# Kernel tuning notes

Measured on AMD Instinct MI355X. Metric: run time of the kernel, lower is better.

Reference implementation:

```python
import jax, jax.numpy as jnp
import numpy as np

B, S, D, H = 2, 2048, 1024, 16
DK = D // H


def setup_inputs() -> dict:
    key = jax.random.key(0)
    ks = jax.random.split(key, 11)
    scale = 1.0 / np.sqrt(D)
    inp = {
        "query": jax.random.normal(ks[0], (B, S, D), dtype=jnp.float32),
        "key": jax.random.normal(ks[1], (B, S, D), dtype=jnp.float32),
        "value": jax.random.normal(ks[2], (B, S, D), dtype=jnp.float32),
        "Wq": jax.random.normal(ks[3], (D, D), dtype=jnp.float32) * scale,
        "bq": jnp.zeros((D,), dtype=jnp.float32),
        "Wk": jax.random.normal(ks[4], (D, D), dtype=jnp.float32) * scale,
        "bk": jnp.zeros((D,), dtype=jnp.float32),
        "Wv": jax.random.normal(ks[5], (D, D), dtype=jnp.float32) * scale,
        "bv": jnp.zeros((D,), dtype=jnp.float32),
        "Wo": jax.random.normal(ks[6], (D, D), dtype=jnp.float32) * scale,
        "bo": jnp.zeros((D,), dtype=jnp.float32),
    }
    return inp


def _split_heads(x):
    # [B,S,D] -> [B,H,S,DK]
    b, s, _ = x.shape
    return x.reshape(b, s, H, DK).transpose(0, 2, 1, 3)


def reference(query, key, value, Wq, bq, Wk, bk, Wv, bv, Wo, bo):
    q = _split_heads(query @ Wq.T + bq)
    k = _split_heads(key @ Wk.T + bk)
    v = _split_heads(value @ Wv.T + bv)
    # scaled dot-product attention: [B,H,S,S]
    scores = jnp.einsum("bhqd,bhkd->bhqk", q, k) / np.sqrt(DK).astype(np.float32)
    attn = jax.nn.softmax(scores, axis=-1)  # stable max-subtract softmax, same math
    ctx = jnp.einsum("bhqk,bhkd->bhqd", attn, v)  # [B,H,S,DK]
    ctx = ctx.transpose(0, 2, 1, 3).reshape(query.shape[0], -1, H * DK)
    return ctx @ Wo.T + bo
```

## Files before the change

kernel.cpp:

```cpp
#include <hip/hip_runtime.h>
#include <math.h>

constexpr int NB = 2;
constexpr int NS = 2048;
constexpr int ND = 1024;
constexpr int NH = 16;
constexpr int NDK = 64;

typedef __attribute__((ext_vector_type(8))) short short8;
typedef __attribute__((ext_vector_type(4))) float floatx4;

__device__ inline unsigned short f2bf(float x) {
    unsigned u = __builtin_bit_cast(unsigned, x);
    u += 0x7fffu + ((u >> 16) & 1u);
    return (unsigned short)(u >> 16);
}

__device__ inline uint4 pack8(float4 a, float4 b) {
    unsigned short t[8] = {f2bf(a.x), f2bf(a.y), f2bf(a.z), f2bf(a.w),
                           f2bf(b.x), f2bf(b.y), f2bf(b.z), f2bf(b.w)};
    return *(uint4*)t;
}

#define GLOAD_LDS16(g, l) __builtin_amdgcn_global_load_lds( \
    (const __attribute__((address_space(1))) void*)(g),     \
    (__attribute__((address_space(3))) void*)(l), 16, 0, 0)

#define QSCALE 0.18033688f

__global__ __launch_bounds__(256) void cvt_all(
    const float* __restrict__ s0, const float* __restrict__ s1,
    const float* __restrict__ s2, const float* __restrict__ s3,
    const float* __restrict__ s4, const float* __restrict__ s5,
    const float* __restrict__ s6,
    unsigned short* __restrict__ d0, unsigned short* __restrict__ d1,
    unsigned short* __restrict__ d2, unsigned short* __restrict__ d3,
    unsigned short* __restrict__ d4, unsigned short* __restrict__ d5,
    unsigned short* __restrict__ d6)
{
    const int y = blockIdx.y;
    const float* srcs[7] = {s0, s1, s2, s3, s4, s5, s6};
    unsigned short* dsts[7] = {d0, d1, d2, d3, d4, d5, d6};
    const int nel = (y < 3) ? NB * NS * ND : ND * ND;
    int i = (blockIdx.x * 256 + threadIdx.x) * 8;
    if (i >= nel) return;
    const float* s = srcs[y];
    unsigned short* d = dsts[y];
    float4 a = *(const float4*)(s + i);
    float4 b = *(const float4*)(s + i + 4);
    *(uint4*)(d + i) = pack8(a, b);
}

__global__ __launch_bounds__(256) void gemm_qkv(
    const unsigned short* __restrict__ Xq, const unsigned short* __restrict__ Xk,
    const unsigned short* __restrict__ Xv,
    const unsigned short* __restrict__ Wq, const unsigned short* __restrict__ Wk,
    const unsigned short* __restrict__ Wv,
    const float* __restrict__ bq, const float* __restrict__ bk,
    const float* __restrict__ bv,
    unsigned short* __restrict__ Cq, unsigned short* __restrict__ Ck,
    unsigned short* __restrict__ Cv)
{
    __shared__ unsigned short As[128 * 32];
    __shared__ unsigned short Bs[128 * 32];
    const int tid = threadIdx.x, w = tid >> 6, lane = tid & 63;
    const int lo = lane & 15, quad = lane >> 4;
    const int bid = blockIdx.x;
    const int seg = bid >> 8;
    const int wi  = bid & 255;
    const int xcd = wi & 7;
    const int t   = wi >> 3;
    const int K = ND;

    int bm, bn;
    const unsigned short *A, *Bw;
    const float* bias;
    if (seg == 2) {
        bm = t & 7; bn = (t >> 3) * 8 + xcd;
        A = Wv; Bw = Xv; bias = bv;
    } else {
        bn = t & 7; bm = (t >> 3) * 8 + xcd;
        if (seg == 1) { A = Xk; Bw = Wk; bias = bk; }
        else          { A = Xq; Bw = Wq; bias = bq; }
    }

    const int wm = (w >> 1) * 64, wn = (w & 1) * 64;

    const int srow = tid >> 2;
    const int sch = (tid & 3) ^ (srow & 3);
    const unsigned short* Ag0 = A + (size_t)(bm * 128 + srow) * K + sch * 8;
    const unsigned short* Ag1 = Ag0 + (size_t)64 * K;
    const unsigned short* Bg0 = Bw + (size_t)(bn * 128 + srow) * K + sch * 8;
    const unsigned short* Bg1 = Bg0 + (size_t)64 * K;
    unsigned short* AsD0 = As + tid * 8;
    unsigned short* AsD1 = As + (tid + 256) * 8;
    unsigned short* BsD0 = Bs + tid * 8;
    unsigned short* BsD1 = Bs + (tid + 256) * 8;

    floatx4 acc[4][4];
    #pragma unroll
    for (int i = 0; i < 4; ++i)
        #pragma unroll
        for (int j = 0; j < 4; ++j) acc[i][j] = (floatx4){0.f, 0.f, 0.f, 0.f};

    const int rpos = (quad ^ (lo & 3)) * 8;

    for (int k0 = 0; k0 < K; k0 += 32) {
        GLOAD_LDS16(Ag0 + k0, AsD0);
        GLOAD_LDS16(Ag1 + k0, AsD1);
        GLOAD_LDS16(Bg0 + k0, BsD0);
        GLOAD_LDS16(Bg1 + k0, BsD1);
        __syncthreads();

        short8 af[4], bf[4];
        #pragma unroll
        for (int i = 0; i < 4; ++i)
            af[i] = *(const short8*)(As + (wm + i * 16 + lo) * 32 + rpos);
        #pragma unroll
        for (int j = 0; j < 4; ++j)
            bf[j] = *(const short8*)(Bs + (wn + j * 16 + lo) * 32 + rpos);

        #pragma unroll
        for (int i = 0; i < 4; ++i)
            #pragma unroll
            for (int j = 0; j < 4; ++j)
                acc[i][j] = __builtin_amdgcn_mfma_f32_16x16x32_bf16(af[i], bf[j], acc[i][j], 0, 0, 0);
        __syncthreads();
    }

    if (seg < 2) {
        unsigned short* C = seg ? Ck : Cq;
        const float scale = seg ? 1.f : QSCALE;
        #pragma unroll
        for (int j = 0; j < 4; ++j) {
            const int col = bn * 128 + wn + j * 16 + lo;
            const float bb = bias[col];
            #pragma unroll
            for (int i = 0; i < 4; ++i)
                #pragma unroll
                for (int r = 0; r < 4; ++r) {
                    const int row = bm * 128 + wm + i * 16 + quad * 4 + r;
                    C[(size_t)row * ND + col] = f2bf((acc[i][j][r] + bb) * scale);
                }
        }
    } else {
        #pragma unroll
        for (int i = 0; i < 4; ++i)
            #pragma unroll
            for (int r = 0; r < 4; ++r) {
                const int row = bm * 128 + wm + i * 16 + quad * 4 + r;
                const float bb = bias[row];
                #pragma unroll
                for (int j = 0; j < 4; ++j) {
                    const int col = bn * 128 + wn + j * 16 + lo;
                    const int b = col >> 11, s = col & (NS - 1);
                    Cv[(size_t)(b * ND + row) * NS + s] = f2bf(acc[i][j][r] + bb);
                }
            }
    }
}

constexpr int PRS = 72;

__global__ __launch_bounds__(256, 4) void attn_mfma(
    const unsigned short* __restrict__ qb,
    const unsigned short* __restrict__ kb,
    const unsigned short* __restrict__ vt,
    float* __restrict__ cacc0, float* __restrict__ cacc1,
    float* __restrict__ lbuf)
{
    __shared__ unsigned short Ks[64 * 64];
    __shared__ unsigned short Vs[64 * 64];
    __shared__ unsigned short Pt[4][32 * PRS];

    const int tid = threadIdx.x, w = tid >> 6, lane = tid & 63;
    const int lo = lane & 15, quad = lane >> 4;
    const int bid = blockIdx.x;
    const int xcd = bid & 7;
    const int tt  = bid >> 3;
    const int qgrp = tt & 15;
    const int bhk  = (tt >> 4) * 8 + xcd;
    const int bh = bhk >> 1, ksp = bhk & 1;
    const int b = bh >> 4, h = bh & 15;
    const int q0 = qgrp * 128 + w * 32;

    short8 qf[2][2];
    #pragma unroll
    for (int qt = 0; qt < 2; ++qt) {
        const unsigned short* qrow =
            qb + (size_t)(b * NS + q0 + qt * 16 + lo) * ND + h * NDK + quad * 8;
        qf[qt][0] = *(const short8*)(qrow);
        qf[qt][1] = *(const short8*)(qrow + 32);
    }

    const int c0 = tid, c1 = tid + 256;
    const int r0 = c0 >> 3, g0 = (c0 & 7) ^ (r0 & 7);
    const int r1 = c1 >> 3, g1 = (c1 & 7) ^ (r1 & 7);
    const unsigned short* Ksrc0 = kb + (size_t)(b * NS + r0) * ND + h * NDK + g0 * 8;
    const unsigned short* Ksrc1 = kb + (size_t)(b * NS + r1) * ND + h * NDK + g1 * 8;
    const unsigned short* Vsrc0 = vt + (size_t)(bh * NDK + r0) * NS + g0 * 8;
    const unsigned short* Vsrc1 = vt + (size_t)(bh * NDK + r1) * NS + g1 * 8;
    unsigned short* Kd0 = Ks + c0 * 8;
    unsigned short* Kd1 = Ks + c1 * 8;
    unsigned short* Vd0 = Vs + c0 * 8;
    unsigned short* Vd1 = Vs + c1 * 8;

    floatx4 acc[2][4], lacc[2];
    #pragma unroll
    for (int qt = 0; qt < 2; ++qt) {
        lacc[qt] = (floatx4){0.f, 0.f, 0.f, 0.f};
        #pragma unroll
        for (int cb = 0; cb < 4; ++cb) acc[qt][cb] = (floatx4){0.f, 0.f, 0.f, 0.f};
    }

    const short8 ones = {0x3F80, 0x3F80, 0x3F80, 0x3F80,
                         0x3F80, 0x3F80, 0x3F80, 0x3F80};
    unsigned short* pw = &Pt[w][0];
    const int pos0 = (quad ^ (lo & 7)) * 8;
    const int pos1 = ((4 + quad) ^ (lo & 7)) * 8;

    for (int key0 = ksp * 1024; key0 < ksp * 1024 + 1024; key0 += 64) {
        GLOAD_LDS16(Ksrc0 + (size_t)key0 * ND, Kd0);
        GLOAD_LDS16(Ksrc1 + (size_t)key0 * ND, Kd1);
        GLOAD_LDS16(Vsrc0 + key0, Vd0);
        GLOAD_LDS16(Vsrc1 + key0, Vd1);
        __syncthreads();

        floatx4 s[2][4];
        #pragma unroll
        for (int t = 0; t < 4; ++t) {
            const int rw = (t * 16 + lo) * 64;
            const short8 kf0 = *(const short8*)(Ks + rw + pos0);
            const short8 kf1 = *(const short8*)(Ks + rw + pos1);
            #pragma unroll
            for (int qt = 0; qt < 2; ++qt) {
                s[qt][t] = __builtin_amdgcn_mfma_f32_16x16x32_bf16(
                    kf0, qf[qt][0], (floatx4){0.f, 0.f, 0.f, 0.f}, 0, 0, 0);
                s[qt][t] = __builtin_amdgcn_mfma_f32_16x16x32_bf16(
                    kf1, qf[qt][1], s[qt][t], 0, 0, 0);
            }
        }

        #pragma unroll
        for (int qt = 0; qt < 2; ++qt)
            #pragma unroll
            for (int t = 0; t < 4; ++t) {
                unsigned u0 = __builtin_bit_cast(unsigned, __builtin_amdgcn_exp2f(s[qt][t][0]));
                unsigned u1 = __builtin_bit_cast(unsigned, __builtin_amdgcn_exp2f(s[qt][t][1]));
                unsigned u2 = __builtin_bit_cast(unsigned, __builtin_amdgcn_exp2f(s[qt][t][2]));
                unsigned u3 = __builtin_bit_cast(unsigned, __builtin_amdgcn_exp2f(s[qt][t][3]));
                uint2 pk = {(u0 >> 16) | (u1 & 0xFFFF0000u),
                            (u2 >> 16) | (u3 & 0xFFFF0000u)};
                *(uint2*)(pw + (qt * 16 + lo) * PRS + t * 16 + quad * 4) = pk;
            }

        short8 pf[2][2];
        #pragma unroll
        for (int qt = 0; qt < 2; ++qt) {
            pf[qt][0] = *(const short8*)(pw + (qt * 16 + lo) * PRS + quad * 8);
            pf[qt][1] = *(const short8*)(pw + (qt * 16 + lo) * PRS + 32 + quad * 8);
            lacc[qt] = __builtin_amdgcn_mfma_f32_16x16x32_bf16(pf[qt][0], ones, lacc[qt], 0, 0, 0);
            lacc[qt] = __builtin_amdgcn_mfma_f32_16x16x32_bf16(pf[qt][1], ones, lacc[qt], 0, 0, 0);
        }

        #pragma unroll
        for (int cb = 0; cb < 4; ++cb) {
            const int rw = (cb * 16 + lo) * 64;
            const short8 vf0 = *(const short8*)(Vs + rw + pos0);
            const short8 vf1 = *(const short8*)(Vs + rw + pos1);
            #pragma unroll
            for (int qt = 0; qt < 2; ++qt) {
                acc[qt][cb] = __builtin_amdgcn_mfma_f32_16x16x32_bf16(pf[qt][0], vf0, acc[qt][cb], 0, 0, 0);
                acc[qt][cb] = __builtin_amdgcn_mfma_f32_16x16x32_bf16(pf[qt][1], vf1, acc[qt][cb], 0, 0, 0);
            }
        }
        __syncthreads();
    }

    float* ca = ksp ? cacc1 : cacc0;
    float* lb = lbuf + (size_t)ksp * (NB * NH * NS);
    #pragma unroll
    for (int qt = 0; qt < 2; ++qt) {
        #pragma unroll
        for (int cb = 0; cb < 4; ++cb)
            #pragma unroll
            for (int r = 0; r < 4; ++r) {
                size_t off = (size_t)(b * NS + q0 + qt * 16 + quad * 4 + r) * ND
                           + h * NDK + cb * 16 + lo;
                ca[off] = acc[qt][cb][r];
            }
        if (lo == 0)
            #pragma unroll
            for (int r = 0; r < 4; ++r)
                lb[(size_t)bh * NS + q0 + qt * 16 + quad * 4 + r] = lacc[qt][r];
    }
}

__global__ __launch_bounds__(256) void gemm_o(
    const float* __restrict__ cacc0, const float* __restrict__ cacc1,
    const float* __restrict__ lbuf, const unsigned short* __restrict__ Bw,
    const float* __restrict__ bias, float* __restrict__ Cout)
{
    __shared__ unsigned short As[64 * 64];
    __shared__ unsigned short Bs[128 * 64];
    const int tid = threadIdx.x, w = tid >> 6, lane = tid & 63;
    const int lo = lane & 15, quad = lane >> 4;
    const int bid = blockIdx.x;
    const int xcd = bid & 7;
    const int tt  = bid >> 3;
    const int bn  = tt & 7;
    const int bm  = (tt >> 3) * 8 + xcd;
    const int K = ND;
    const int wm = (w >> 1) * 32, wn = (w & 1) * 64;
    const size_t LHALF = (size_t)NB * NH * NS;

    const int ar = tid >> 3;
    const int ag = (tid & 7) ^ (ar & 7);
    const int tok0 = bm * 64 + ar, tok1 = tok0 + 32;
    const float* A00 = cacc0 + (size_t)tok0 * ND + ag * 8;
    const float* A01 = cacc1 + (size_t)tok0 * ND + ag * 8;
    const float* A10 = cacc0 + (size_t)tok1 * ND + ag * 8;
    const float* A11 = cacc1 + (size_t)tok1 * ND + ag * 8;
    const size_t lb0 = (size_t)((tok0 >> 11) << 4) * NS + (tok0 & (NS - 1));
    const size_t lb1 = (size_t)((tok1 >> 11) << 4) * NS + (tok1 & (NS - 1));
    unsigned short* AsD0 = As + tid * 8;
    unsigned short* AsD1 = As + (tid + 256) * 8;

    const unsigned short* Bg[4];
    unsigned short* BsD[4];
    #pragma unroll
    for (int p = 0; p < 4; ++p) {
        int c = tid + 256 * p, r = c >> 3, g = (c & 7) ^ (r & 7);
        Bg[p] = Bw + (size_t)(bn * 128 + r) * K + g * 8;
        BsD[p] = Bs + c * 8;
    }

    floatx4 acc[2][4];
    #pragma unroll
    for (int i = 0; i < 2; ++i)
        #pragma unroll
        for (int j = 0; j < 4; ++j) acc[i][j] = (floatx4){0.f, 0.f, 0.f, 0.f};

    float4 ra[8];
    float lv0, lv1;
    ra[0] = *(const float4*)(A00);     ra[1] = *(const float4*)(A00 + 4);
    ra[2] = *(const float4*)(A01);     ra[3] = *(const float4*)(A01 + 4);
    ra[4] = *(const float4*)(A10);     ra[5] = *(const float4*)(A10 + 4);
    ra[6] = *(const float4*)(A11);     ra[7] = *(const float4*)(A11 + 4);
    lv0 = lbuf[lb0] + lbuf[lb0 + LHALF];
    lv1 = lbuf[lb1] + lbuf[lb1 + LHALF];

    for (int k0 = 0; k0 < K; k0 += 64) {
        const float inv0 = __builtin_amdgcn_rcpf(lv0);
        const float inv1 = __builtin_amdgcn_rcpf(lv1);
        __syncthreads();
        #pragma unroll
        for (int p = 0; p < 4; ++p) GLOAD_LDS16(Bg[p] + k0, BsD[p]);
        {
            float4 s0 = {(ra[0].x + ra[2].x) * inv0, (ra[0].y + ra[2].y) * inv0,
                         (ra[0].z + ra[2].z) * inv0, (ra[0].w + ra[2].w) * inv0};
            float4 s1 = {(ra[1].x + ra[3].x) * inv0, (ra[1].y + ra[3].y) * inv0,
                         (ra[1].z + ra[3].z) * inv0, (ra[1].w + ra[3].w) * inv0};
            *(uint4*)AsD0 = pack8(s0, s1);
            float4 s2 = {(ra[4].x + ra[6].x) * inv1, (ra[4].y + ra[6].y) * inv1,
                         (ra[4].z + ra[6].z) * inv1, (ra[4].w + ra[6].w) * inv1};
            float4 s3 = {(ra[5].x + ra[7].x) * inv1, (ra[5].y + ra[7].y) * inv1,
                         (ra[5].z + ra[7].z) * inv1, (ra[5].w + ra[7].w) * inv1};
            *(uint4*)AsD1 = pack8(s2, s3);
        }
        __syncthreads();

        const int kn = k0 + 64;
        if (kn < K) {
            ra[0] = *(const float4*)(A00 + kn); ra[1] = *(const float4*)(A00 + kn + 4);
            ra[2] = *(const float4*)(A01 + kn); ra[3] = *(const float4*)(A01 + kn + 4);
            ra[4] = *(const float4*)(A10 + kn); ra[5] = *(const float4*)(A10 + kn + 4);
            ra[6] = *(const float4*)(A11 + kn); ra[7] = *(const float4*)(A11 + kn + 4);
            const size_t hoff = (size_t)(kn >> 6) * NS;
            lv0 = lbuf[lb0 + hoff] + lbuf[lb0 + hoff + LHALF];
            lv1 = lbuf[lb1 + hoff] + lbuf[lb1 + hoff + LHALF];
        }

        #pragma unroll
        for (int s = 0; s < 2; ++s) {
            const int pos = ((s * 4 + quad) ^ (lo & 7)) * 8;
            short8 af[2], bf[4];
            #pragma unroll
            for (int i = 0; i < 2; ++i)
                af[i] = *(const short8*)(As + (wm + i * 16 + lo) * 64 + pos);
            #pragma unroll
            for (int j = 0; j < 4; ++j)
                bf[j] = *(const short8*)(Bs + (wn + j * 16 + lo) * 64 + pos);
            #pragma unroll
            for (int i = 0; i < 2; ++i)
                #pragma unroll
                for (int j = 0; j < 4; ++j)
                    acc[i][j] = __builtin_amdgcn_mfma_f32_16x16x32_bf16(af[i], bf[j], acc[i][j], 0, 0, 0);
        }
    }

    #pragma unroll
    for (int j = 0; j < 4; ++j) {
        const int col = bn * 128 + wn + j * 16 + lo;
        const float bb = bias[col];
        #pragma unroll
        for (int i = 0; i < 2; ++i)
            #pragma unroll
            for (int r = 0; r < 4; ++r) {
                const int row = bm * 64 + wm + i * 16 + quad * 4 + r;
                Cout[(size_t)row * ND + col] = acc[i][j][r] + bb;
            }
    }
}

extern "C" void kernel_launch(void* const* d_in, const int* in_sizes, int n_in,
                              void* d_out, int out_size, void* d_ws, size_t ws_size,
                              hipStream_t stream)
{
    const float* query = (const float*)d_in[0];
    const float* key   = (const float*)d_in[1];
    const float* value = (const float*)d_in[2];
    const float* Wq    = (const float*)d_in[3];
    const float* bq    = (const float*)d_in[4];
    const float* Wk    = (const float*)d_in[5];
    const float* bk    = (const float*)d_in[6];
    const float* Wv    = (const float*)d_in[7];
    const float* bv    = (const float*)d_in[8];
    const float* Wo    = (const float*)d_in[9];
    const float* bo    = (const float*)d_in[10];
    float* out = (float*)d_out;

    const size_t n  = (size_t)NB * NS * ND;
    const size_t nw = (size_t)ND * ND;

    unsigned short* X0   = (unsigned short*)d_ws;
    unsigned short* X1   = X0 + n;
    unsigned short* X2   = X1 + n;
    unsigned short* W0   = X2 + n;
    unsigned short* W1   = W0 + nw;
    unsigned short* W2   = W1 + nw;
    unsigned short* W3   = W2 + nw;
    unsigned short* qbuf = W3 + nw;
    unsigned short* kbuf = qbuf + n;
    unsigned short* vtb  = kbuf + n;
    float* cacc1 = (float*)(vtb + n);
    float* lbuf  = cacc1 + n;
    float* cacc0 = (float*)X1;

    const int M = NB * NS;

    cvt_all<<<dim3((int)(n / 2048), 7), 256, 0, stream>>>(
        query, key, value, Wq, Wk, Wv, Wo, X0, X1, X2, W0, W1, W2, W3);

    gemm_qkv<<<768, 256, 0, stream>>>(X0, X1, X2, W0, W1, W2,
                                      bq, bk, bv, qbuf, kbuf, vtb);

    attn_mfma<<<1024, 256, 0, stream>>>(qbuf, kbuf, vtb, cacc0, cacc1, lbuf);

    gemm_o<<<512, 256, 0, stream>>>(cacc0, cacc1, lbuf, W3, bo, out);
}
```

Measured before the change: 231.0 us.

## Triple-buffer LDS tiles in QKV projection GEMM with async prefetch

The QKV projection GEMM now uses three LDS stages and issues global-to-LDS loads two k-steps ahead. Partial vmcnt waits replace full __syncthreads, so memory latency can overlap with MFMA work. This triples the GEMM's LDS footprint to 48KB, which may reduce occupancy. It also depends on hand-written waitcnt values matching the exact number of outstanding loads.

```diff
diff --git a/kernel.cpp b/kernel.cpp
--- a/kernel.cpp
+++ b/kernel.cpp
@@ -61,8 +61,8 @@
     unsigned short* __restrict__ Cq, unsigned short* __restrict__ Ck,
     unsigned short* __restrict__ Cv)
 {
-    __shared__ unsigned short As[128 * 32];
-    __shared__ unsigned short Bs[128 * 32];
+    __shared__ unsigned short As[3][128 * 32];
+    __shared__ unsigned short Bs[3][128 * 32];
     const int tid = threadIdx.x, w = tid >> 6, lane = tid & 63;
     const int lo = lane & 15, quad = lane >> 4;
     const int bid = blockIdx.x;
@@ -92,10 +92,7 @@
     const unsigned short* Ag1 = Ag0 + (size_t)64 * K;
     const unsigned short* Bg0 = Bw + (size_t)(bn * 128 + srow) * K + sch * 8;
     const unsigned short* Bg1 = Bg0 + (size_t)64 * K;
-    unsigned short* AsD0 = As + tid * 8;
-    unsigned short* AsD1 = As + (tid + 256) * 8;
-    unsigned short* BsD0 = Bs + tid * 8;
-    unsigned short* BsD1 = Bs + (tid + 256) * 8;
+    const int ld0 = tid * 8, ld1 = (tid + 256) * 8;
 
     floatx4 acc[4][4];
     #pragma unroll
@@ -105,27 +102,52 @@
 
     const int rpos = (quad ^ (lo & 3)) * 8;
 
+    GLOAD_LDS16(Ag0,      &As[0][ld0]);
+    GLOAD_LDS16(Ag1,      &As[0][ld1]);
+    GLOAD_LDS16(Bg0,      &Bs[0][ld0]);
+    GLOAD_LDS16(Bg1,      &Bs[0][ld1]);
+    GLOAD_LDS16(Ag0 + 32, &As[1][ld0]);
+    GLOAD_LDS16(Ag1 + 32, &As[1][ld1]);
+    GLOAD_LDS16(Bg0 + 32, &Bs[1][ld0]);
+    GLOAD_LDS16(Bg1 + 32, &Bs[1][ld1]);
+
+    int cur = 0;
     for (int k0 = 0; k0 < K; k0 += 32) {
-        GLOAD_LDS16(Ag0 + k0, AsD0);
-        GLOAD_LDS16(Ag1 + k0, AsD1);
-        GLOAD_LDS16(Bg0 + k0, BsD0);
-        GLOAD_LDS16(Bg1 + k0, BsD1);
-        __syncthreads();
-
+        const int kp = k0 + 64;
+        int nxt = cur + 2; if (nxt >= 3) nxt -= 3;
+        if (kp < K) {
+            GLOAD_LDS16(Ag0 + kp, &As[nxt][ld0]);
+            GLOAD_LDS16(Ag1 + kp, &As[nxt][ld1]);
+            GLOAD_LDS16(Bg0 + kp, &Bs[nxt][ld0]);
+            GLOAD_LDS16(Bg1 + kp, &Bs[nxt][ld1]);
+            asm volatile("s_waitcnt vmcnt(8)" ::: "memory");
+        } else if (k0 + 32 < K) {
+            asm volatile("s_waitcnt vmcnt(4)" ::: "memory");
+        } else {
+            asm volatile("s_waitcnt vmcnt(0)" ::: "memory");
+        }
+        __builtin_amdgcn_s_barrier();
+        __builtin_amdgcn_sched_barrier(0);
+
+        const unsigned short* CA = As[cur];
+        const unsigned short* CB = Bs[cur];
         short8 af[4], bf[4];
         #pragma unroll
         for (int i = 0; i < 4; ++i)
-            af[i] = *(const short8*)(As + (wm + i * 16 + lo) * 32 + rpos);
+            af[i] = *(const short8*)(CA + (wm + i * 16 + lo) * 32 + rpos);
         #pragma unroll
         for (int j = 0; j < 4; ++j)
-            bf[j] = *(const short8*)(Bs + (wn + j * 16 + lo) * 32 + rpos);
+            bf[j] = *(const short8*)(CB + (wn + j * 16 + lo) * 32 + rpos);
 
         #pragma unroll
         for (int i = 0; i < 4; ++i)
             #pragma unroll
             for (int j = 0; j < 4; ++j)
                 acc[i][j] = __builtin_amdgcn_mfma_f32_16x16x32_bf16(af[i], bf[j], acc[i][j], 0, 0, 0);
-        __syncthreads();
+
+        __builtin_amdgcn_sched_barrier(0);
+        __builtin_amdgcn_s_barrier();
+        cur = cur + 1; if (cur == 3) cur = 0;
     }
 
     if (seg < 2) {
```

Result: no change. 235.3 us (+1.9%).

## Rewrite QKV GEMM as 256x256 double-buffered 8-wave pipelined kernel

Applied to the files above, without the earlier changes.

The QKV projection GEMM moves from 128x128 tiles with a K-step of 32 and one LDS buffer to 256x256 tiles with a K-step of 64, using 512 threads and double-buffered LDS. Global-to-LDS loads for later K tiles are interleaved with MFMA phases, using explicit vmcnt waits, barriers and s_setprio. The aim is to hide load latency and raise arithmetic intensity per block. In exchange, the grid shrinks to 192 blocks, which is fewer than the CU count, and LDS use and register pressure grow.

```diff
diff --git a/kernel.cpp b/kernel.cpp
--- a/kernel.cpp
+++ b/kernel.cpp
@@ -51,7 +51,22 @@
     *(uint4*)(d + i) = pack8(a, b);
 }
 
-__global__ __launch_bounds__(256) void gemm_qkv(
+template<int QA, int QB>
+__device__ __forceinline__ void mfma_quad(
+    floatx4 (&acc)[8][4], const short8 (&ta)[4][2], const short8 (&tb)[2][2][2])
+{
+#pragma unroll
+    for (int ii = 0; ii < 4; ++ii)
+#pragma unroll
+        for (int jj = 0; jj < 2; ++jj) {
+            acc[QA * 4 + ii][QB * 2 + jj] = __builtin_amdgcn_mfma_f32_16x16x32_bf16(
+                ta[ii][0], tb[QB][jj][0], acc[QA * 4 + ii][QB * 2 + jj], 0, 0, 0);
+            acc[QA * 4 + ii][QB * 2 + jj] = __builtin_amdgcn_mfma_f32_16x16x32_bf16(
+                ta[ii][1], tb[QB][jj][1], acc[QA * 4 + ii][QB * 2 + jj], 0, 0, 0);
+        }
+}
+
+__global__ __launch_bounds__(512, 2) void gemm_qkv(
     const unsigned short* __restrict__ Xq, const unsigned short* __restrict__ Xk,
     const unsigned short* __restrict__ Xv,
     const unsigned short* __restrict__ Wq, const unsigned short* __restrict__ Wk,
@@ -61,98 +76,150 @@
     unsigned short* __restrict__ Cq, unsigned short* __restrict__ Ck,
     unsigned short* __restrict__ Cv)
 {
-    __shared__ unsigned short As[128 * 32];
-    __shared__ unsigned short Bs[128 * 32];
+    __shared__ unsigned short As[2][256 * 64];
+    __shared__ unsigned short Bs[2][256 * 64];
+
     const int tid = threadIdx.x, w = tid >> 6, lane = tid & 63;
     const int lo = lane & 15, quad = lane >> 4;
     const int bid = blockIdx.x;
-    const int seg = bid >> 8;
-    const int wi  = bid & 255;
-    const int xcd = wi & 7;
-    const int t   = wi >> 3;
+    const int seg = bid >> 6;
+    const int idx = bid & 63;
+    const int xcd = idx & 7;
+    const int t8  = idx >> 3;
     const int K = ND;
 
     int bm, bn;
     const unsigned short *A, *Bw;
     const float* bias;
     if (seg == 2) {
-        bm = t & 7; bn = (t >> 3) * 8 + xcd;
+        bm = t8 & 3; bn = (t8 >> 2) * 8 + xcd;
         A = Wv; Bw = Xv; bias = bv;
     } else {
-        bn = t & 7; bm = (t >> 3) * 8 + xcd;
+        bn = t8 & 3; bm = (t8 >> 2) * 8 + xcd;
         if (seg == 1) { A = Xk; Bw = Wk; bias = bk; }
         else          { A = Xq; Bw = Wq; bias = bq; }
     }
 
-    const int wm = (w >> 1) * 64, wn = (w & 1) * 64;
-
-    const int srow = tid >> 2;
-    const int sch = (tid & 3) ^ (srow & 3);
-    const unsigned short* Ag0 = A + (size_t)(bm * 128 + srow) * K + sch * 8;
-    const unsigned short* Ag1 = Ag0 + (size_t)64 * K;
-    const unsigned short* Bg0 = Bw + (size_t)(bn * 128 + srow) * K + sch * 8;
-    const unsigned short* Bg1 = Bg0 + (size_t)64 * K;
-    unsigned short* AsD0 = As + tid * 8;
-    unsigned short* AsD1 = As + (tid + 256) * 8;
-    unsigned short* BsD0 = Bs + tid * 8;
-    unsigned short* BsD1 = Bs + (tid + 256) * 8;
-
-    floatx4 acc[4][4];
-    #pragma unroll
-    for (int i = 0; i < 4; ++i)
-        #pragma unroll
+    const int WM = (w >> 2) * 128, WN = (w & 3) * 64;
+
+    const int srow = tid >> 3;
+    const int sgo  = ((tid & 7) ^ (srow & 7)) * 8;
+    const unsigned short* Asrc = A  + (size_t)(bm * 256 + srow) * K + sgo;
+    const unsigned short* Bsrc = Bw + (size_t)(bn * 256 + srow) * K + sgo;
+
+#define SA(bf_, t_, s_) GLOAD_LDS16(Asrc + (size_t)(s_) * 64 * K + (t_) * 64, \
+                                    &As[bf_][(s_) * 4096 + tid * 8])
+#define SB(bf_, t_, s_) GLOAD_LDS16(Bsrc + (size_t)(s_) * 64 * K + (t_) * 64, \
+                                    &Bs[bf_][(s_) * 4096 + tid * 8])
+
+    const int rp0 = ((quad) ^ (lo & 7)) * 8;
+    const int rp1 = ((4 + quad) ^ (lo & 7)) * 8;
+
+    short8 ta[4][2], tb[2][2][2];
+
+#define RDA(bf_, qa_) { _Pragma("unroll") \
+    for (int ii = 0; ii < 4; ++ii) { \
+        const unsigned short* p_ = &As[bf_][(WM + (qa_) * 64 + ii * 16 + lo) * 64]; \
+        ta[ii][0] = *(const short8*)(p_ + rp0); \
+        ta[ii][1] = *(const short8*)(p_ + rp1); } }
+#define RDB(bf_, qb_) { _Pragma("unroll") \
+    for (int jj = 0; jj < 2; ++jj) { \
+        const unsigned short* p_ = &Bs[bf_][(WN + (qb_) * 32 + jj * 16 + lo) * 64]; \
+        tb[qb_][jj][0] = *(const short8*)(p_ + rp0); \
+        tb[qb_][jj][1] = *(const short8*)(p_ + rp1); } }
+
+#define PH_SYNC1 __builtin_amdgcn_s_barrier(); \
+    asm volatile("s_waitcnt lgkmcnt(0)" ::: "memory"); \
+    __builtin_amdgcn_sched_barrier(0); \
+    __builtin_amdgcn_s_setprio(1);
+#define PH_SYNC2 __builtin_amdgcn_s_setprio(0); \
+    __builtin_amdgcn_sched_barrier(0); \
+    __builtin_amdgcn_s_barrier();
+
+    floatx4 acc[8][4];
+#pragma unroll
+    for (int i = 0; i < 8; ++i)
+#pragma unroll
         for (int j = 0; j < 4; ++j) acc[i][j] = (floatx4){0.f, 0.f, 0.f, 0.f};
 
-    const int rpos = (quad ^ (lo & 3)) * 8;
-
-    for (int k0 = 0; k0 < K; k0 += 32) {
-        GLOAD_LDS16(Ag0 + k0, AsD0);
-        GLOAD_LDS16(Ag1 + k0, AsD1);
-        GLOAD_LDS16(Bg0 + k0, BsD0);
-        GLOAD_LDS16(Bg1 + k0, BsD1);
-        __syncthreads();
-
-        short8 af[4], bf[4];
-        #pragma unroll
-        for (int i = 0; i < 4; ++i)
-            af[i] = *(const short8*)(As + (wm + i * 16 + lo) * 32 + rpos);
-        #pragma unroll
-        for (int j = 0; j < 4; ++j)
-            bf[j] = *(const short8*)(Bs + (wn + j * 16 + lo) * 32 + rpos);
-
-        #pragma unroll
-        for (int i = 0; i < 4; ++i)
-            #pragma unroll
-            for (int j = 0; j < 4; ++j)
-                acc[i][j] = __builtin_amdgcn_mfma_f32_16x16x32_bf16(af[i], bf[j], acc[i][j], 0, 0, 0);
-        __syncthreads();
-    }
+    SB(0, 0, 0); SB(0, 0, 1); SB(0, 0, 2); SB(0, 0, 3);
+    SA(0, 0, 0); SA(0, 0, 1); SA(0, 0, 2); SA(0, 0, 3);
+    SB(1, 1, 0); SB(1, 1, 1); SB(1, 1, 2); SB(1, 1, 3);
+    asm volatile("s_waitcnt vmcnt(4)" ::: "memory");
+    __builtin_amdgcn_s_barrier();
+
+    constexpr int NIT = ND / 128;
+#pragma unroll 1
+    for (int it = 0; it < NIT; ++it) {
+        const bool nl = (it < NIT - 1);
+        const int t1 = 2 * it + 1, t2 = 2 * it + 2, t3 = 2 * it + 3;
+
+        RDA(0, 0); RDB(0, 0);
+        SA(1, t1, 0); SA(1, t1, 1);
+        PH_SYNC1; mfma_quad<0, 0>(acc, ta, tb); PH_SYNC2;
+
+        RDB(0, 1);
+        SA(1, t1, 2); SA(1, t1, 3);
+        PH_SYNC1; mfma_quad<0, 1>(acc, ta, tb); PH_SYNC2;
+
+        RDA(0, 1);
+        if (nl) { SB(0, t2, 0); SB(0, t2, 1); }
+        PH_SYNC1; mfma_quad<1, 1>(acc, ta, tb); PH_SYNC2;
+
+        if (nl) { SB(0, t2, 2); SB(0, t2, 3); }
+        if (nl) asm volatile("s_waitcnt vmcnt(4)" ::: "memory");
+        else    asm volatile("s_waitcnt vmcnt(0)" ::: "memory");
+        PH_SYNC1; mfma_quad<1, 0>(acc, ta, tb); PH_SYNC2;
+
+        RDA(1, 0); RDB(1, 0);
+        if (nl) { SA(0, t2, 0); SA(0, t2, 1); }
+        PH_SYNC1; mfma_quad<0, 0>(acc, ta, tb); PH_SYNC2;
+
+        RDB(1, 1);
+        if (nl) { SA(0, t2, 2); SA(0, t2, 3); }
+        PH_SYNC1; mfma_quad<0, 1>(acc, ta, tb); PH_SYNC2;
+
+        RDA(1, 1);
+        if (nl) { SB(1, t3, 0); SB(1, t3, 1); }
+        PH_SYNC1; mfma_quad<1, 1>(acc, ta, tb); PH_SYNC2;
+
+        if (nl) { SB(1, t3, 2); SB(1, t3, 3); }
+        if (nl) asm volatile("s_waitcnt vmcnt(4)" ::: "memory");
+        PH_SYNC1; mfma_quad<1, 0>(acc, ta, tb); PH_SYNC2;
+    }
+
+#undef SA
+#undef SB
+#undef RDA
+#undef RDB
+#undef PH_SYNC1
+#undef PH_SYNC2
 
     if (seg < 2) {
         unsigned short* C = seg ? Ck : Cq;
         const float scale = seg ? 1.f : QSCALE;
-        #pragma unroll
+#pragma unroll
         for (int j = 0; j < 4; ++j) {
-            const int col = bn * 128 + wn + j * 16 + lo;
+            const int col = bn * 256 + WN + j * 16 + lo;
             const float bb = bias[col];
-            #pragma unroll
-            for (int i = 0; i < 4; ++i)
-                #pragma unroll
+#pragma unroll
+            for (int i = 0; i < 8; ++i)
+#pragma unroll
                 for (int r = 0; r < 4; ++r) {
-                    const int row = bm * 128 + wm + i * 16 + quad * 4 + r;
+                    const int row = bm * 256 + WM + i * 16 + quad * 4 + r;
                     C[(size_t)row * ND + col] = f2bf((acc[i][j][r] + bb) * scale);
                 }
         }
     } else {
-        #pragma unroll
-        for (int i = 0; i < 4; ++i)
-            #pragma unroll
+#pragma unroll
+        for (int i = 0; i < 8; ++i)
+#pragma unroll
             for (int r = 0; r < 4; ++r) {
-                const int row = bm * 128 + wm + i * 16 + quad * 4 + r;
+                const int row = bm * 256 + WM + i * 16 + quad * 4 + r;
                 const float bb = bias[row];
-                #pragma unroll
+#pragma unroll
                 for (int j = 0; j < 4; ++j) {
-                    const int col = bn * 128 + wn + j * 16 + lo;
+                    const int col = bn * 256 + WN + j * 16 + lo;
                     const int b = col >> 11, s = col & (NS - 1);
                     Cv[(size_t)(b * ND + row) * NS + s] = f2bf(acc[i][j][r] + bb);
                 }
@@ -447,12 +514,10 @@
     float* lbuf  = cacc1 + n;
     float* cacc0 = (float*)X1;
 
-    const int M = NB * NS;
-
     cvt_all<<<dim3((int)(n / 2048), 7), 256, 0, stream>>>(
         query, key, value, Wq, Wk, Wv, Wo, X0, X1, X2, W0, W1, W2, W3);
 
-    gemm_qkv<<<768, 256, 0, stream>>>(X0, X1, X2, W0, W1, W2,
+    gemm_qkv<<<192, 512, 0, stream>>>(X0, X1, X2, W0, W1, W2,
                                       bq, bk, bv, qbuf, kbuf, vtb);
 
     attn_mfma<<<1024, 256, 0, stream>>>(qbuf, kbuf, vtb, cacc0, cacc1, lbuf);
```

New measurement: 222.0 us. 3.9% less time.
